# Performance work log

Hardware: AMD Instinct MI355X
Metric: run time of the kernel (lower is better)

Reference implementation:

```python
import jax, jax.numpy as jnp
import numpy as np

WEIGHT = 1000.0      # start/end cell penalty
LONELY_W = 15.0      # cell lit outside cluster
CLUSTER_W = 5.0      # cell unlit inside cluster
CELL_W = 20.0        # cell on a shortest manhattan path
CSIZE_W = 12.0       # cluster-size penalty
GAP_W = 300.0        # gap-to-endpoint penalty
H = W = 10


def _md(y1, x1, y2, x2):
    return jnp.abs(y1 - y2) + jnp.abs(x1 - x2)


def _per_sample(result, points):
    # result: [H, W] float, points: [2, 2] int (row, col) of start and end
    p0y, p0x = points[0, 0], points[0, 1]
    p1y, p1x = points[1, 0], points[1, 1]
    base = _md(p0y, p0x, p1y, p1x)

    loss_start = (2.0 - (result[p0y, p0x] + result[p1y, p1x])) * WEIGHT

    # 8-connected flood fill from start over cells whose value rounds to 1.
    mask = jnp.round(result) == 1.0
    seed = jnp.zeros((H, W), bool).at[p0y, p0x].set(True)

    def dilate(_, c):
        p = jnp.pad(c, 1)
        nb = (p[:-2, :-2] | p[:-2, 1:-1] | p[:-2, 2:] |
              p[1:-1, :-2] | p[1:-1, 2:] |
              p[2:, :-2] | p[2:, 1:-1] | p[2:, 2:])
        return c | (nb & mask)

    # 8-connected diameter of a 10x10 grid is 9; H+W iterations is a safe bound.
    cluster = jax.lax.fori_loop(0, H + W, dilate, seed)

    rows = jnp.arange(H)[:, None]
    cols = jnp.arange(W)[None, :]

    # per-cell manhattan detour penalty
    d2 = _md(rows, cols, p0y, p0x) + _md(rows, cols, p1y, p1x)
    delta = (d2 - base).astype(result.dtype)
    single_cell = jnp.sum(jnp.where(delta == 0.0,
                                    (1.0 - result) * CELL_W,
                                    result * delta * 0.5))

    # NB: the original tests [column, row] membership against [row, col]
    # cluster entries -> transposed membership map. Faithfully reproduced.
    in_cl = cluster.T
    csize = jnp.sum(cluster).astype(result.dtype)
    lonelyness = jnp.sum(jnp.where(in_cl, (1.0 - result) * CLUSTER_W,
                                   result * LONELY_W))
    cluster_size_pen = jnp.sum(jnp.where(in_cl, result * csize * CSIZE_W, 0.0))

    # nearest cluster cell to the end point (strict improvement over base)
    dist_end = _md(rows, cols, p1y, p1x)
    masked = jnp.where(cluster, dist_end, H * W + 10).reshape(-1)
    idx = jnp.argmin(masked)
    minval = masked[idx]
    better = minval < base
    ny = jnp.where(better, idx // W, p0y)
    nx = jnp.where(better, idx % W, p0x)
    gap = jnp.minimum(base, minval)

    oy = p1y - ny
    ox = p1x - nx

    def upd(cond, cy, cx, st):
        by, bx, bg = st
        d = _md(cy, cx, p1y, p1x)
        b = cond & (d < bg)
        return (jnp.where(b, cy, by), jnp.where(b, cx, bx), jnp.where(b, d, bg))

    st = (ny, nx, gap)
    c = ox < 0
    st = upd(c, ny, nx - 1, st)
    st = upd(c & (ny != 0), ny - 1, nx - 1, st)
    st = upd(c & (ny != H - 1), ny + 1, nx - 1, st)
    c = ox > 0
    st = upd(c, ny, nx + 1, st)
    st = upd(c & (ny != 0), ny - 1, nx + 1, st)
    st = upd(c & (ny != H - 1), ny + 1, nx + 1, st)
    st = upd(oy < 0, ny - 1, nx, st)
    st = upd(oy > 0, ny + 1, nx, st)
    ncy = jnp.clip(st[0], 0, H - 1)
    ncx = jnp.clip(st[1], 0, W - 1)

    gap_pen = gap.astype(result.dtype) * GAP_W * (1.0 - result[ncy, ncx])

    return loss_start + lonelyness + single_cell + cluster_size_pen + gap_pen


def setup_inputs() -> dict:
    key = jax.random.key(0)
    k1, k2 = jax.random.split(key)
    B = 262144
    result_given = jax.random.uniform(k1, (B, 1, H, W), dtype=jnp.float32)
    points_given = jax.random.randint(k2, (B, 2, 2), 0, 10, dtype=jnp.int64 if jax.config.jax_enable_x64 else jnp.int32)
    return {"result_given": result_given, "points_given": points_given}


def reference(result_given, points_given):
    losses = jax.vmap(_per_sample)(result_given[:, 0], points_given)
    return jnp.sum(losses).reshape(1)
```

## Files before the change

kernel.cpp:

```cpp
#include <hip/hip_runtime.h>
#include <cstdint>

#define GH 10
#define GW 10

__device__ __forceinline__ void gld_lds16(const float4* g, float4* l)
{
    __builtin_amdgcn_global_load_lds(
        (const __attribute__((address_space(1))) void*)g,
        (__attribute__((address_space(3))) void*)l,
        16 , 0 , 0 );
}

__global__ __launch_bounds__(256, 3) void custom_loss_kernel(
    const float* __restrict__ result,
    const int* __restrict__ points,
    float* __restrict__ out,
    int B)
{
    __shared__ float lds[4 * 3200];
    __shared__ float wsum[4];
    const int tix = threadIdx.x;
    const int lane = tix & 63;
    const int wid = tix >> 6;
    const int h = tix & 1;
    const int t = lane >> 1;

    const int s = blockIdx.x * 128 + wid * 32 + t;
    float* __restrict__ myLds = lds + wid * 3200;

    {
        const size_t wb4 = ((size_t)blockIdx.x * 128 + wid * 32) * 25;
        const size_t total4 = (size_t)B * 25;
        const float4* __restrict__ g4 = (const float4*)result;
        float4* l4 = (float4*)myLds;
#pragma unroll
        for (int k = 0; k < 12; ++k) {
            size_t gi = wb4 + k * 64 + lane;
            if (gi >= total4) gi = total4 - 1;
            gld_lds16(g4 + gi, l4 + k * 64);
        }
        if (lane < 32) {
            size_t gi = wb4 + 768 + lane;
            if (gi >= total4) gi = total4 - 1;
            l4[768 + lane] = g4[gi];
        }
        asm volatile("s_waitcnt vmcnt(0) lgkmcnt(0)" ::: "memory");
    }

    float loss = 0.f;
    if (s < B) {
        const int4 p = ((const int4*)points)[s];
        const int p0y = p.x, p0x = p.y, p1y = p.z, p1x = p.w;
        const int dy0 = abs(p0y - p1y), dx0 = abs(p0x - p1x);
        const int base0 = dy0 + dx0;
        const int idx0 = p0y * GW + p0x;
        const int idx1 = p1y * GW + p1x;

        const float* __restrict__ sp = myLds + t * 100;
        const float rs = sp[idx0];
        const float re = sp[idx1];

        float adxf[10], inboxf[10];
#pragma unroll
        for (int x = 0; x < 10; ++x) {
            const int a = abs(x - p0x) + abs(x - p1x) - dx0;
            adxf[x] = (float)a;
            inboxf[x] = (a == 0) ? 1.f : 0.f;
        }

        const float2* __restrict__ rp2 = (const float2*)(sp + h * 50);
        float sum_h = 0.f, sc_h = 0.f, box_h = 0.f;
        uint64_t mword = 0;
#pragma unroll
        for (int i = 0; i < 5; ++i) {
            const int y = 5 * h + i;
            float v[10];
#pragma unroll
            for (int j2 = 0; j2 < 5; ++j2) {
                const float2 tt = rp2[i * 5 + j2];
                v[2 * j2] = tt.x; v[2 * j2 + 1] = tt.y;
            }
            const float rowacc = ((v[0]+v[1])+(v[2]+v[3])) +
                                 ((v[4]+v[5])+(v[6]+v[7])) + (v[8]+v[9]);
            sum_h += rowacc;
            const int ay = abs(y - p0y) + abs(y - p1y) - dy0;
            sc_h = fmaf((float)ay, rowacc, sc_h);
            float boxrow = 0.f;
            uint32_t rm = 0u;
#pragma unroll
            for (int x = 0; x < 10; ++x) {
                sc_h = fmaf(adxf[x], v[x], sc_h);
                boxrow = fmaf(inboxf[x], v[x], boxrow);
                rm |= (v[x] > 0.5f) ? (1u << x) : 0u;
            }
            box_h += (ay == 0) ? boxrow : 0.f;
            mword |= (uint64_t)rm << (10 * i);
        }
        const float sum_all = sum_h + __shfl_xor(sum_h, 1);
        const float sc      = sc_h  + __shfl_xor(sc_h, 1);
        const float boxSum  = box_h + __shfl_xor(box_h, 1);
        const uint64_t mo = (uint64_t)__shfl_xor((unsigned long long)mword, 1);
        const uint64_t mlo = h ? mo : mword;
        const uint64_t mhi = h ? mword : mo;

        const uint64_t M50 = (1ull << 50) - 1;
        const uint64_t C0  = 0x10040100401ull;
        const uint64_t NC0 = M50 & ~C0;
        const uint64_t NC9 = M50 & ~(C0 << 9);
        uint64_t clo = 0, chi = 0;
        if (idx0 < 50) clo = 1ull << idx0; else chi = 1ull << (idx0 - 50);
#pragma unroll 1
        for (int it = 0; it < GH + GW; ++it) {
            const uint64_t hlo = clo | ((clo << 1) & NC0) | ((clo >> 1) & NC9);
            const uint64_t hhi = chi | ((chi << 1) & NC0) | ((chi >> 1) & NC9);
            uint64_t nlo = (hlo | (hlo << 10) | (hlo >> 10) | ((hhi & 0x3FFull) << 40)) & mlo;
            uint64_t nhi = (hhi | (hhi << 10) | (hhi >> 10) | (hlo >> 40)) & mhi;
            nlo |= clo; nhi |= chi;
            if (nlo == clo && nhi == chi) break;
            clo = nlo; chi = nhi;
        }
        const int K = __popcll(clo) + __popcll(chi);

        const uint64_t wlo = clo >> (5 * h);
        const uint64_t whi = chi >> (5 * h);
        uint32_t fld[10];
#pragma unroll
        for (int x = 0; x < 10; ++x) {
            const uint64_t w = (x < 5) ? wlo : whi;
            fld[x] = (uint32_t)((w >> ((x % 5) * 10)) & 0x1Full);
        }
        float st_h = 0.f;
#pragma unroll
        for (int i = 0; i < 5; ++i) {
            float v[10];
#pragma unroll
            for (int j2 = 0; j2 < 5; ++j2) {
                const float2 tt = rp2[i * 5 + j2];
                v[2 * j2] = tt.x; v[2 * j2 + 1] = tt.y;
            }
#pragma unroll
            for (int x = 0; x < 10; ++x) {
                const uint32_t bit = (fld[x] >> i) & 1u;
                st_h = fmaf((float)bit, v[x], st_h);
            }
        }
        const float S_T = st_h + __shfl_xor(st_h, 1);

        int bestd = 1000, bidx = 0;
        const uint64_t cw = h ? chi : clo;
#pragma unroll
        for (int i = 0; i < 5; ++i) {
            const int y = 5 * h + i;
            const uint32_t rb = (uint32_t)((cw >> (10 * i)) & 0x3FFull);
            const uint32_t left  = rb & ((2u << p1x) - 1);
            const uint32_t right = rb >> p1x;
            const int dl = left  ? (p1x - (31 - __builtin_clz(left))) : 1000;
            const int dr = right ? __builtin_ctz(right) : 1000;
            int dx, xx;
            if (dl <= dr) { dx = dl; xx = p1x - dl; }
            else          { dx = dr; xx = p1x + dr; }
            const int d = abs(y - p1y) + dx;
            if (rb && d < bestd) { bestd = d; bidx = y * GW + xx; }
        }
        {
            const int od = __shfl_xor(bestd, 1);
            const int oi = __shfl_xor(bidx, 1);
            if (od < bestd || (od == bestd && oi < bidx)) { bestd = od; bidx = oi; }
        }

        const bool better = bestd < base0;
        const int ny = better ? bidx / 10 : p0y;
        const int nx = better ? bidx % 10 : p0x;
        const int gap = min(base0, bestd);

        int by = ny, bx = nx, bg = gap;
        const int oy = p1y - ny, ox = p1x - nx;
        auto upd = [&](bool cond, int cy, int cx) {
            const int d = abs(cy - p1y) + abs(cx - p1x);
            if (cond && (d < bg)) { by = cy; bx = cx; bg = d; }
        };
        upd(ox < 0,                     ny,     nx - 1);
        upd((ox < 0) && (ny != 0),      ny - 1, nx - 1);
        upd((ox < 0) && (ny != GH - 1), ny + 1, nx - 1);
        upd(ox > 0,                     ny,     nx + 1);
        upd((ox > 0) && (ny != 0),      ny - 1, nx + 1);
        upd((ox > 0) && (ny != GH - 1), ny + 1, nx + 1);
        upd(oy < 0,                     ny - 1, nx);
        upd(oy > 0,                     ny + 1, nx);
        const int ncy = min(max(by, 0), GH - 1);
        const int ncx = min(max(bx, 0), GW - 1);
        const float rn = sp[ncy * GW + ncx];

        const float csf = (float)K;
        const float nboxf = (float)((dy0 + 1) * (dx0 + 1));
        const float loss_start = (2.f - (rs + re)) * 1000.f;
        const float lon = 5.f * csf + 15.f * sum_all - 20.f * S_T;
        const float single_cell = 0.5f * sc + 20.f * (nboxf - boxSum);
        const float cpen = 12.f * csf * S_T;
        const float gap_pen = (float)gap * 300.f * (1.f - rn);
        loss = loss_start + lon + single_cell + cpen + gap_pen;
        if (h != 0) loss = 0.f;
    }

#pragma unroll
    for (int off = 32; off > 0; off >>= 1)
        loss += __shfl_down(loss, off);
    if (lane == 0) wsum[wid] = loss;
    __syncthreads();
    if (tix == 0)
        atomicAdd(out, wsum[0] + wsum[1] + wsum[2] + wsum[3]);
}

extern "C" void kernel_launch(void* const* d_in, const int* in_sizes, int n_in,
                              void* d_out, int out_size, void* d_ws, size_t ws_size,
                              hipStream_t stream)
{
    const float* result = (const float*)d_in[0];
    const int* points   = (const int*)d_in[1];
    float* out = (float*)d_out;
    const int B = in_sizes[0] / 100;
    hipMemsetAsync(out, 0, sizeof(float), stream);
    const int block = 256;
    const int grid = (2 * B + block - 1) / block;
    custom_loss_kernel<<<grid, block, 0, stream>>>(result, points, out, B);
}
```

Measured before the change: 164.9 us.

## Double-buffer LDS staging so each wave processes four sample chunks

Each wave now handles 128 samples in four chunks of 32. The next chunk's grid data and points are prefetched into an alternate LDS buffer through async global-to-LDS loads while the current chunk is computed. Per-sample math moves into a helper function. The block shrinks to 128 threads, each wave atomically adds its own partial sum, and the block-level shared reduction and barrier are removed. The aim is to hide global-load latency behind compute. The cost is about 53 KB of LDS per block, which leaves fewer resident waves per CU and a coarser tail across the grid.

```diff
diff --git a/kernel.cpp b/kernel.cpp
--- a/kernel.cpp
+++ b/kernel.cpp
@@ -12,204 +12,225 @@
         16 , 0 , 0 );
 }
 
-__global__ __launch_bounds__(256, 3) void custom_loss_kernel(
+__device__ __forceinline__ float sample_loss(
+    const float* __restrict__ sp, const int4 p, const int h)
+{
+    const int p0y = p.x, p0x = p.y, p1y = p.z, p1x = p.w;
+    const int dy0 = abs(p0y - p1y), dx0 = abs(p0x - p1x);
+    const int base0 = dy0 + dx0;
+    const int idx0 = p0y * GW + p0x;
+    const int idx1 = p1y * GW + p1x;
+
+    const float rs = sp[idx0];
+    const float re = sp[idx1];
+
+    float adxf[10], inboxf[10];
+#pragma unroll
+    for (int x = 0; x < 10; ++x) {
+        const int a = abs(x - p0x) + abs(x - p1x) - dx0;
+        adxf[x] = (float)a;
+        inboxf[x] = (a == 0) ? 1.f : 0.f;
+    }
+
+    const float2* __restrict__ rp2 = (const float2*)(sp + h * 50);
+    float sum_h = 0.f, sc_h = 0.f, box_h = 0.f;
+    uint64_t mword = 0;
+#pragma unroll
+    for (int i = 0; i < 5; ++i) {
+        const int y = 5 * h + i;
+        float v[10];
+#pragma unroll
+        for (int j2 = 0; j2 < 5; ++j2) {
+            const float2 tt = rp2[i * 5 + j2];
+            v[2 * j2] = tt.x; v[2 * j2 + 1] = tt.y;
+        }
+        const float rowacc = ((v[0]+v[1])+(v[2]+v[3])) +
+                             ((v[4]+v[5])+(v[6]+v[7])) + (v[8]+v[9]);
+        sum_h += rowacc;
+        const int ay = abs(y - p0y) + abs(y - p1y) - dy0;
+        sc_h = fmaf((float)ay, rowacc, sc_h);
+        float boxrow = 0.f;
+        uint32_t rm = 0u;
+#pragma unroll
+        for (int x = 0; x < 10; ++x) {
+            sc_h = fmaf(adxf[x], v[x], sc_h);
+            boxrow = fmaf(inboxf[x], v[x], boxrow);
+            rm |= (v[x] > 0.5f) ? (1u << x) : 0u;
+        }
+        box_h += (ay == 0) ? boxrow : 0.f;
+        mword |= (uint64_t)rm << (10 * i);
+    }
+    const float sum_all = sum_h + __shfl_xor(sum_h, 1);
+    const float sc      = sc_h  + __shfl_xor(sc_h, 1);
+    const float boxSum  = box_h + __shfl_xor(box_h, 1);
+    const uint64_t mo = (uint64_t)__shfl_xor((unsigned long long)mword, 1);
+    const uint64_t mlo = h ? mo : mword;
+    const uint64_t mhi = h ? mword : mo;
+
+    const uint64_t M50 = (1ull << 50) - 1;
+    const uint64_t C0  = 0x10040100401ull;
+    const uint64_t NC0 = M50 & ~C0;
+    const uint64_t NC9 = M50 & ~(C0 << 9);
+    uint64_t clo = 0, chi = 0;
+    if (idx0 < 50) clo = 1ull << idx0; else chi = 1ull << (idx0 - 50);
+#pragma unroll 1
+    for (int it = 0; it < GH + GW; ++it) {
+        const uint64_t hlo = clo | ((clo << 1) & NC0) | ((clo >> 1) & NC9);
+        const uint64_t hhi = chi | ((chi << 1) & NC0) | ((chi >> 1) & NC9);
+        uint64_t nlo = (hlo | (hlo << 10) | (hlo >> 10) | ((hhi & 0x3FFull) << 40)) & mlo;
+        uint64_t nhi = (hhi | (hhi << 10) | (hhi >> 10) | (hlo >> 40)) & mhi;
+        nlo |= clo; nhi |= chi;
+        if (nlo == clo && nhi == chi) break;
+        clo = nlo; chi = nhi;
+    }
+    const int K = __popcll(clo) + __popcll(chi);
+
+    const uint64_t wlo = clo >> (5 * h);
+    const uint64_t whi = chi >> (5 * h);
+    uint32_t fld[10];
+#pragma unroll
+    for (int x = 0; x < 10; ++x) {
+        const uint64_t w = (x < 5) ? wlo : whi;
+        fld[x] = (uint32_t)((w >> ((x % 5) * 10)) & 0x1Full);
+    }
+    float st_h = 0.f;
+#pragma unroll
+    for (int i = 0; i < 5; ++i) {
+        float v[10];
+#pragma unroll
+        for (int j2 = 0; j2 < 5; ++j2) {
+            const float2 tt = rp2[i * 5 + j2];
+            v[2 * j2] = tt.x; v[2 * j2 + 1] = tt.y;
+        }
+#pragma unroll
+        for (int x = 0; x < 10; ++x) {
+            const uint32_t bit = (fld[x] >> i) & 1u;
+            st_h = fmaf((float)bit, v[x], st_h);
+        }
+    }
+    const float S_T = st_h + __shfl_xor(st_h, 1);
+
+    int bestd = 1000, bidx = 0;
+    const uint64_t cw = h ? chi : clo;
+#pragma unroll
+    for (int i = 0; i < 5; ++i) {
+        const int y = 5 * h + i;
+        const uint32_t rb = (uint32_t)((cw >> (10 * i)) & 0x3FFull);
+        const uint32_t left  = rb & ((2u << p1x) - 1);
+        const uint32_t right = rb >> p1x;
+        const int dl = left  ? (p1x - (31 - __builtin_clz(left))) : 1000;
+        const int dr = right ? __builtin_ctz(right) : 1000;
+        int dx, xx;
+        if (dl <= dr) { dx = dl; xx = p1x - dl; }
+        else          { dx = dr; xx = p1x + dr; }
+        const int d = abs(y - p1y) + dx;
+        if (rb && d < bestd) { bestd = d; bidx = y * GW + xx; }
+    }
+    {
+        const int od = __shfl_xor(bestd, 1);
+        const int oi = __shfl_xor(bidx, 1);
+        if (od < bestd || (od == bestd && oi < bidx)) { bestd = od; bidx = oi; }
+    }
+
+    const bool better = bestd < base0;
+    const int ny = better ? bidx / 10 : p0y;
+    const int nx = better ? bidx % 10 : p0x;
+    const int gap = min(base0, bestd);
+
+    int by = ny, bx = nx, bg = gap;
+    const int oy = p1y - ny, ox = p1x - nx;
+    auto upd = [&](bool cond, int cy, int cx) {
+        const int d = abs(cy - p1y) + abs(cx - p1x);
+        if (cond && (d < bg)) { by = cy; bx = cx; bg = d; }
+    };
+    upd(ox < 0,                     ny,     nx - 1);
+    upd((ox < 0) && (ny != 0),      ny - 1, nx - 1);
+    upd((ox < 0) && (ny != GH - 1), ny + 1, nx - 1);
+    upd(ox > 0,                     ny,     nx + 1);
+    upd((ox > 0) && (ny != 0),      ny - 1, nx + 1);
+    upd((ox > 0) && (ny != GH - 1), ny + 1, nx + 1);
+    upd(oy < 0,                     ny - 1, nx);
+    upd(oy > 0,                     ny + 1, nx);
+    const int ncy = min(max(by, 0), GH - 1);
+    const int ncx = min(max(bx, 0), GW - 1);
+    const float rn = sp[ncy * GW + ncx];
+
+    const float csf = (float)K;
+    const float nboxf = (float)((dy0 + 1) * (dx0 + 1));
+    const float loss_start = (2.f - (rs + re)) * 1000.f;
+    const float lon = 5.f * csf + 15.f * sum_all - 20.f * S_T;
+    const float single_cell = 0.5f * sc + 20.f * (nboxf - boxSum);
+    const float cpen = 12.f * csf * S_T;
+    const float gap_pen = (float)gap * 300.f * (1.f - rn);
+    return loss_start + lon + single_cell + cpen + gap_pen;
+}
+
+__global__ __launch_bounds__(128) void custom_loss_kernel(
     const float* __restrict__ result,
     const int* __restrict__ points,
     float* __restrict__ out,
     int B)
 {
-    __shared__ float lds[4 * 3200];
-    __shared__ float wsum[4];
+    __shared__ float lds[2 * 2 * 3328];
     const int tix = threadIdx.x;
     const int lane = tix & 63;
     const int wid = tix >> 6;
     const int h = tix & 1;
     const int t = lane >> 1;
 
-    const int s = blockIdx.x * 128 + wid * 32 + t;
-    float* __restrict__ myLds = lds + wid * 3200;
-
-    {
-        const size_t wb4 = ((size_t)blockIdx.x * 128 + wid * 32) * 25;
-        const size_t total4 = (size_t)B * 25;
-        const float4* __restrict__ g4 = (const float4*)result;
-        float4* l4 = (float4*)myLds;
-#pragma unroll
-        for (int k = 0; k < 12; ++k) {
-            size_t gi = wb4 + k * 64 + lane;
+    const int waveBase = (blockIdx.x * 2 + wid) * 128;
+    float* __restrict__ bufA = lds + wid * 6656;
+    float* __restrict__ bufB = bufA + 3328;
+
+    const size_t total4 = (size_t)B * 25;
+    const float4* __restrict__ g4 = (const float4*)result;
+    const int4* __restrict__ pts4 = (const int4*)points;
+
+    auto stage = [&](int c, float* dstf) {
+        float4* dst = (float4*)dstf;
+        const size_t cb4 = ((size_t)waveBase + (size_t)c * 32) * 25;
+#pragma unroll
+        for (int k = 0; k < 13; ++k) {
+            size_t gi = cb4 + (size_t)(k * 64 + lane);
             if (gi >= total4) gi = total4 - 1;
-            gld_lds16(g4 + gi, l4 + k * 64);
-        }
-        if (lane < 32) {
-            size_t gi = wb4 + 768 + lane;
-            if (gi >= total4) gi = total4 - 1;
-            l4[768 + lane] = g4[gi];
-        }
+            gld_lds16(g4 + gi, dst + k * 64);
+        }
+    };
+    auto ploadi = [&](int c) -> int4 {
+        int si = waveBase + c * 32 + t;
+        if (si >= B) si = B - 1;
+        return pts4[si];
+    };
+
+    stage(0, bufA);
+    int4 pts_next = ploadi(0);
+
+    float wacc = 0.f;
+#pragma unroll 1
+    for (int c = 0; c < 4; ++c) {
         asm volatile("s_waitcnt vmcnt(0) lgkmcnt(0)" ::: "memory");
-    }
-
-    float loss = 0.f;
-    if (s < B) {
-        const int4 p = ((const int4*)points)[s];
-        const int p0y = p.x, p0x = p.y, p1y = p.z, p1x = p.w;
-        const int dy0 = abs(p0y - p1y), dx0 = abs(p0x - p1x);
-        const int base0 = dy0 + dx0;
-        const int idx0 = p0y * GW + p0x;
-        const int idx1 = p1y * GW + p1x;
-
-        const float* __restrict__ sp = myLds + t * 100;
-        const float rs = sp[idx0];
-        const float re = sp[idx1];
-
-        float adxf[10], inboxf[10];
-#pragma unroll
-        for (int x = 0; x < 10; ++x) {
-            const int a = abs(x - p0x) + abs(x - p1x) - dx0;
-            adxf[x] = (float)a;
-            inboxf[x] = (a == 0) ? 1.f : 0.f;
-        }
-
-        const float2* __restrict__ rp2 = (const float2*)(sp + h * 50);
-        float sum_h = 0.f, sc_h = 0.f, box_h = 0.f;
-        uint64_t mword = 0;
-#pragma unroll
-        for (int i = 0; i < 5; ++i) {
-            const int y = 5 * h + i;
-            float v[10];
-#pragma unroll
-            for (int j2 = 0; j2 < 5; ++j2) {
-                const float2 tt = rp2[i * 5 + j2];
-                v[2 * j2] = tt.x; v[2 * j2 + 1] = tt.y;
-            }
-            const float rowacc = ((v[0]+v[1])+(v[2]+v[3])) +
-                                 ((v[4]+v[5])+(v[6]+v[7])) + (v[8]+v[9]);
-            sum_h += rowacc;
-            const int ay = abs(y - p0y) + abs(y - p1y) - dy0;
-            sc_h = fmaf((float)ay, rowacc, sc_h);
-            float boxrow = 0.f;
-            uint32_t rm = 0u;
-#pragma unroll
-            for (int x = 0; x < 10; ++x) {
-                sc_h = fmaf(adxf[x], v[x], sc_h);
-                boxrow = fmaf(inboxf[x], v[x], boxrow);
-                rm |= (v[x] > 0.5f) ? (1u << x) : 0u;
-            }
-            box_h += (ay == 0) ? boxrow : 0.f;
-            mword |= (uint64_t)rm << (10 * i);
-        }
-        const float sum_all = sum_h + __shfl_xor(sum_h, 1);
-        const float sc      = sc_h  + __shfl_xor(sc_h, 1);
-        const float boxSum  = box_h + __shfl_xor(box_h, 1);
-        const uint64_t mo = (uint64_t)__shfl_xor((unsigned long long)mword, 1);
-        const uint64_t mlo = h ? mo : mword;
-        const uint64_t mhi = h ? mword : mo;
-
-        const uint64_t M50 = (1ull << 50) - 1;
-        const uint64_t C0  = 0x10040100401ull;
-        const uint64_t NC0 = M50 & ~C0;
-        const uint64_t NC9 = M50 & ~(C0 << 9);
-        uint64_t clo = 0, chi = 0;
-        if (idx0 < 50) clo = 1ull << idx0; else chi = 1ull << (idx0 - 50);
-#pragma unroll 1
-        for (int it = 0; it < GH + GW; ++it) {
-            const uint64_t hlo = clo | ((clo << 1) & NC0) | ((clo >> 1) & NC9);
-            const uint64_t hhi = chi | ((chi << 1) & NC0) | ((chi >> 1) & NC9);
-            uint64_t nlo = (hlo | (hlo << 10) | (hlo >> 10) | ((hhi & 0x3FFull) << 40)) & mlo;
-            uint64_t nhi = (hhi | (hhi << 10) | (hhi >> 10) | (hlo >> 40)) & mhi;
-            nlo |= clo; nhi |= chi;
-            if (nlo == clo && nhi == chi) break;
-            clo = nlo; chi = nhi;
-        }
-        const int K = __popcll(clo) + __popcll(chi);
-
-        const uint64_t wlo = clo >> (5 * h);
-        const uint64_t whi = chi >> (5 * h);
-        uint32_t fld[10];
-#pragma unroll
-        for (int x = 0; x < 10; ++x) {
-            const uint64_t w = (x < 5) ? wlo : whi;
-            fld[x] = (uint32_t)((w >> ((x % 5) * 10)) & 0x1Full);
-        }
-        float st_h = 0.f;
-#pragma unroll
-        for (int i = 0; i < 5; ++i) {
-            float v[10];
-#pragma unroll
-            for (int j2 = 0; j2 < 5; ++j2) {
-                const float2 tt = rp2[i * 5 + j2];
-                v[2 * j2] = tt.x; v[2 * j2 + 1] = tt.y;
-            }
-#pragma unroll
-            for (int x = 0; x < 10; ++x) {
-                const uint32_t bit = (fld[x] >> i) & 1u;
-                st_h = fmaf((float)bit, v[x], st_h);
-            }
-        }
-        const float S_T = st_h + __shfl_xor(st_h, 1);
-
-        int bestd = 1000, bidx = 0;
-        const uint64_t cw = h ? chi : clo;
-#pragma unroll
-        for (int i = 0; i < 5; ++i) {
-            const int y = 5 * h + i;
-            const uint32_t rb = (uint32_t)((cw >> (10 * i)) & 0x3FFull);
-            const uint32_t left  = rb & ((2u << p1x) - 1);
-            const uint32_t right = rb >> p1x;
-            const int dl = left  ? (p1x - (31 - __builtin_clz(left))) : 1000;
-            const int dr = right ? __builtin_ctz(right) : 1000;
-            int dx, xx;
-            if (dl <= dr) { dx = dl; xx = p1x - dl; }
-            else          { dx = dr; xx = p1x + dr; }
-            const int d = abs(y - p1y) + dx;
-            if (rb && d < bestd) { bestd = d; bidx = y * GW + xx; }
-        }
-        {
-            const int od = __shfl_xor(bestd, 1);
-            const int oi = __shfl_xor(bidx, 1);
-            if (od < bestd || (od == bestd && oi < bidx)) { bestd = od; bidx = oi; }
-        }
-
-        const bool better = bestd < base0;
-        const int ny = better ? bidx / 10 : p0y;
-        const int nx = better ? bidx % 10 : p0x;
-        const int gap = min(base0, bestd);
-
-        int by = ny, bx = nx, bg = gap;
-        const int oy = p1y - ny, ox = p1x - nx;
-        auto upd = [&](bool cond, int cy, int cx) {
-            const int d = abs(cy - p1y) + abs(cx - p1x);
-            if (cond && (d < bg)) { by = cy; bx = cx; bg = d; }
-        };
-        upd(ox < 0,                     ny,     nx - 1);
-        upd((ox < 0) && (ny != 0),      ny - 1, nx - 1);
-        upd((ox < 0) && (ny != GH - 1), ny + 1, nx - 1);
-        upd(ox > 0,                     ny,     nx + 1);
-        upd((ox > 0) && (ny != 0),      ny - 1, nx + 1);
-        upd((ox > 0) && (ny != GH - 1), ny + 1, nx + 1);
-        upd(oy < 0,                     ny - 1, nx);
-        upd(oy > 0,                     ny + 1, nx);
-        const int ncy = min(max(by, 0), GH - 1);
-        const int ncx = min(max(bx, 0), GW - 1);
-        const float rn = sp[ncy * GW + ncx];
-
-        const float csf = (float)K;
-        const float nboxf = (float)((dy0 + 1) * (dx0 + 1));
-        const float loss_start = (2.f - (rs + re)) * 1000.f;
-        const float lon = 5.f * csf + 15.f * sum_all - 20.f * S_T;
-        const float single_cell = 0.5f * sc + 20.f * (nboxf - boxSum);
-        const float cpen = 12.f * csf * S_T;
-        const float gap_pen = (float)gap * 300.f * (1.f - rn);
-        loss = loss_start + lon + single_cell + cpen + gap_pen;
-        if (h != 0) loss = 0.f;
-    }
-
-#pragma unroll
-    for (int off = 32; off > 0; off >>= 1)
-        loss += __shfl_down(loss, off);
-    if (lane == 0) wsum[wid] = loss;
-    __syncthreads();
-    if (tix == 0)
-        atomicAdd(out, wsum[0] + wsum[1] + wsum[2] + wsum[3]);
+        const int4 p = pts_next;
+        if (c < 3) {
+            stage(c + 1, (c & 1) ? bufA : bufB);
+            pts_next = ploadi(c + 1);
+        }
+
+        const float* __restrict__ sp =
+            ((c & 1) ? bufB : bufA) + t * 100;
+        const int s = waveBase + c * 32 + t;
+
+        float loss = 0.f;
+        if (s < B) {
+            loss = sample_loss(sp, p, h);
+            if (h != 0) loss = 0.f;
+        }
+#pragma unroll
+        for (int off = 32; off > 0; off >>= 1)
+            loss += __shfl_down(loss, off);
+        wacc += loss;
+    }
+
+    if (lane == 0) atomicAdd(out, wacc);
 }
 
 extern "C" void kernel_launch(void* const* d_in, const int* in_sizes, int n_in,
@@ -221,7 +242,7 @@
     float* out = (float*)d_out;
     const int B = in_sizes[0] / 100;
     hipMemsetAsync(out, 0, sizeof(float), stream);
-    const int block = 256;
-    const int grid = (2 * B + block - 1) / block;
+    const int block = 128;
+    const int grid = (B + 255) / 256;
     custom_loss_kernel<<<grid, block, 0, stream>>>(result, points, out, B);
 }
```

New measurement: 184.9 us. 12.1% more time.
